# Kernel tuning notes

Hardware: AMD Instinct MI355X
Metric: run time of the kernel (lower is better)

The kernel has to match this reference:

```python
import jax, jax.numpy as jnp
import numpy as np

NUM_HEADS = 16
HEAD_DIM = 64
HIDDEN = NUM_HEADS * HEAD_DIM  # 1024
BATCH, SEQ = 4, 2048


def setup_inputs() -> dict:
    key = jax.random.key(0)
    k1, k2, k3, k4 = jax.random.split(key, 4)
    hidden_states = jax.random.normal(k1, (BATCH, SEQ, HIDDEN), dtype=jnp.float32)
    attention_mask = jnp.arange(SEQ)[None, :] < int(SEQ * 0.9)
    attention_mask = jnp.broadcast_to(attention_mask, (BATCH, SEQ))
    s_in = 1.0 / np.sqrt(HIDDEN)
    Wqkv = jax.random.normal(k2, (HIDDEN, 3 * HIDDEN), dtype=jnp.float32) * s_in
    Wout = jax.random.normal(k3, (HIDDEN, HIDDEN), dtype=jnp.float32) * s_in
    bout = jnp.zeros((HIDDEN,), dtype=jnp.float32)
    return {"hidden_states": hidden_states, "attention_mask": attention_mask,
            "Wqkv": Wqkv, "Wout": Wout, "bout": bout}


def reference(hidden_states, attention_mask, Wqkv, Wout, bout):
    B, S, H = hidden_states.shape
    qkv = hidden_states @ Wqkv  # [B,S,3*H]
    qkv = qkv.reshape(B, S, 3, NUM_HEADS, HEAD_DIM)
    qkv = jnp.transpose(qkv, (2, 0, 3, 1, 4))  # [3,B,nh,S,hd]
    q, k, v = qkv[0], qkv[1], qkv[2]
    scale = 1.0 / jnp.sqrt(jnp.float32(HEAD_DIM))
    attn = jnp.einsum('bhid,bhjd->bhij', q, k) * scale  # [B,nh,S,S]
    bias = jnp.where(attention_mask[:, None, None, :], 0.0,
                     jnp.finfo(jnp.float32).min)
    attn = attn + bias
    attn = jax.nn.softmax(attn, axis=-1)
    out = jnp.einsum('bhij,bhjd->bhid', attn, v)  # [B,nh,S,hd]
    out = jnp.transpose(out, (0, 2, 1, 3)).reshape(B, S, H)
    return out @ Wout + bout
```

## Files before the change

### kernel.cpp

```cpp
#include <hip/hip_runtime.h>


typedef short bh8 __attribute__((ext_vector_type(8)));
typedef short bh4 __attribute__((ext_vector_type(4)));
typedef float f32x4 __attribute__((ext_vector_type(4)));

#define B_ 4
#define S_ 2048
#define NH_ 16
#define HD_ 64
#define H_ 1024

__device__ float g_biasf[B_ * S_];
__device__ int g_tl[B_ * 33];
__device__ unsigned g_act[B_];

__device__ inline short f2bf(float f) {
    unsigned u = __builtin_bit_cast(unsigned, f);
    u = (u + 0x7fffu + ((u >> 16) & 1u)) >> 16;
    return (short)u;
}

__device__ inline unsigned pk2bf(float a, float b) {
#if __has_builtin(__builtin_amdgcn_cvt_pk_bf16_f32)
    auto r = __builtin_amdgcn_cvt_pk_bf16_f32(a, b);
    return __builtin_bit_cast(unsigned, r);
#else
    unsigned ua = __builtin_bit_cast(unsigned, a) + 0x8000u;
    unsigned ub = __builtin_bit_cast(unsigned, b) + 0x8000u;
    return __builtin_amdgcn_perm(ub, ua, 0x07060302);
#endif
}

__global__ void prep_all(const float* __restrict__ hidden, const float* __restrict__ Wqkv,
                         const float* __restrict__ Wout, const int* __restrict__ mask,
                         short* __restrict__ Xbf, short* __restrict__ WqkvT,
                         short* __restrict__ WoutT, float qs) {
    __shared__ float tile[32][33];
    int bi = blockIdx.x, tid = threadIdx.x;

    if (bi < 8192) {
        int i = (bi * 256 + tid) * 4;
        float4 v = *(const float4*)(hidden + i);
        union { short s[4]; unsigned long long u; } r;
        r.s[0] = f2bf(v.x); r.s[1] = f2bf(v.y); r.s[2] = f2bf(v.z); r.s[3] = f2bf(v.w);
        *(unsigned long long*)(Xbf + i) = r.u;
        return;
    }
    if (bi < 12288) {
        const float* in; short* out; int N, qcols, idx;
        if (bi < 11264) { in = Wqkv; out = WqkvT; N = 3 * H_; qcols = H_; idx = bi - 8192;
        } else          { in = Wout; out = WoutT; N = H_;    qcols = 0;  idx = bi - 11264; }
        int xt = (bi < 11264) ? 96 : 32;
        int n0 = (idx % xt) * 32, k0 = (idx / xt) * 32;
        int tx = tid & 31, ty = tid >> 5;
#pragma unroll
        for (int i = 0; i < 32; i += 8)
            tile[ty + i][tx] = in[(long)(k0 + ty + i) * N + n0 + tx];
        __syncthreads();
#pragma unroll
        for (int i = 0; i < 32; i += 8) {
            int n = n0 + ty + i;
            float v = tile[tx][ty + i];
            if (n < qcols) v *= qs;
            out[(long)n * H_ + k0 + tx] = f2bf(v);
        }
        return;
    }
    if (bi < 12320) {
        int i = (bi - 12288) * 256 + tid;
        g_biasf[i] = mask[i] ? 0.0f : -1e30f;
        return;
    }
    {
        int b = bi - 12320;
        if (tid < 64) {
            int t = tid, flag = 0;
            if (t < 32) {
                bool anyA = false, anyM = false;
                for (int i = 0; i < 64; ++i) {
                    int m = mask[b * S_ + t * 64 + i];
                    anyA |= (m != 0); anyM |= (m == 0);
                }
                flag = anyA ? (anyM ? 1 : 2) : 0;
            }
            unsigned long long act = __ballot(flag != 0);
            int pos = __popcll(act & ((1ull << t) - 1ull));
            if (flag) g_tl[b * 33 + 1 + pos] = t | (flag << 16);
            if (t == 0) { g_tl[b * 33] = __popcll(act); g_act[b] = (unsigned)act; }
        }
    }
}

__global__ __launch_bounds__(256, 2) void gemm_bf16(
    const short* __restrict__ A, const short* __restrict__ Bt,
    int M, int N, int K, int mode,
    short* __restrict__ qk, short* __restrict__ vt,
    const float* __restrict__ bias, float* __restrict__ out) {
    __shared__ short smem[128 * 136];
    short* sA[2] = { smem, smem + 4096 };
    short* sB[2] = { smem + 8192, smem + 12288 };
    int tid = threadIdx.x;
    int lane = tid & 63, wid = tid >> 6;
    int quad = lane >> 4, l15 = lane & 15;
    int wy = wid >> 1, wx = wid & 1;
    int m0 = blockIdx.y * 128, n0 = blockIdx.x * 128;
    int rsw = ((l15 >> 1) & 3) << 3;

    if (mode == 0 && n0 >= 1024) {
        int b = m0 >> 11, t0 = (m0 & 2047) >> 6;
        if (((g_act[b] >> t0) & 3u) == 0u) return;
    }

    f32x4 acc[4][4] = {};
    const short* Ag = A + (long)m0 * K;
    const short* Bg = Bt + (long)n0 * K;

    for (int k0 = 0; k0 < K; k0 += 64) {
#pragma unroll
        for (int half = 0; half < 2; ++half) {
#pragma unroll
            for (int i = 0; i < 2; ++i) {
                int flat = i * 256 + tid;
                int r = flat >> 2;
                int c = ((flat & 3) ^ ((flat >> 3) & 3)) << 3;
                __builtin_amdgcn_global_load_lds(
                    (const __attribute__((address_space(1))) void*)(Ag + (long)r * K + k0 + half * 32 + c),
                    (__attribute__((address_space(3))) void*)(sA[half] + i * 2048 + wid * 512),
                    16, 0, 0);
                __builtin_amdgcn_global_load_lds(
                    (const __attribute__((address_space(1))) void*)(Bg + (long)r * K + k0 + half * 32 + c),
                    (__attribute__((address_space(3))) void*)(sB[half] + i * 2048 + wid * 512),
                    16, 0, 0);
            }
        }
        __syncthreads();
#pragma unroll
        for (int half = 0; half < 2; ++half) {
            bh8 af[4], bfr[4];
            int qoff = (quad << 3) ^ rsw;
#pragma unroll
            for (int mi = 0; mi < 4; ++mi)
                af[mi] = *(const bh8*)(sA[half] + (wy * 64 + mi * 16 + l15) * 32 + qoff);
#pragma unroll
            for (int ni = 0; ni < 4; ++ni)
                bfr[ni] = *(const bh8*)(sB[half] + (wx * 64 + ni * 16 + l15) * 32 + qoff);
#pragma unroll
            for (int mi = 0; mi < 4; ++mi)
#pragma unroll
                for (int ni = 0; ni < 4; ++ni)
                    acc[mi][ni] = __builtin_amdgcn_mfma_f32_16x16x32_bf16(af[mi], bfr[ni], acc[mi][ni], 0, 0, 0);
        }
        __syncthreads();
    }

    if (mode == 0) {
        bool isV = (n0 >= 2048);
#pragma unroll
        for (int mi = 0; mi < 4; ++mi)
#pragma unroll
            for (int ni = 0; ni < 4; ++ni) {
                int c = wx * 64 + ni * 16 + l15;
                int rb = wy * 64 + mi * 16 + quad * 4;
                if (isV) {
                    unsigned lo = pk2bf(acc[mi][ni][0], acc[mi][ni][1]);
                    unsigned hi = pk2bf(acc[mi][ni][2], acc[mi][ni][3]);
                    uint2 uu = {lo, hi};
                    *(bh4*)(smem + c * 136 + rb) = __builtin_bit_cast(bh4, uu);
                } else {
#pragma unroll
                    for (int reg = 0; reg < 4; ++reg)
                        smem[(rb + reg) * 136 + c] = f2bf(acc[mi][ni][reg]);
                }
            }
        __syncthreads();
        int b = m0 >> 11, sbase = m0 & 2047;
#pragma unroll
        for (int j = 0; j < 8; ++j) {
            int f = (j * 256 + tid) * 8;
            int i0 = f >> 7, i1 = f & 127;
            bh8 v = *(const bh8*)(smem + i0 * 136 + i1);
            if (isV) {
                int cc = n0 - 2048 + i0;
                int h = cc >> 6, d = cc & 63;
                *(bh8*)(vt + ((long)(b * NH_ + h) * HD_ + d) * S_ + sbase + i1) = v;
            } else {
                *(bh8*)(qk + (long)(m0 + i0) * 2048 + n0 + i1) = v;
            }
        }
    } else {
#pragma unroll
        for (int mi = 0; mi < 4; ++mi)
#pragma unroll
            for (int ni = 0; ni < 4; ++ni) {
                int gc = n0 + wx * 64 + ni * 16 + l15;
                float bv = bias[gc];
#pragma unroll
                for (int reg = 0; reg < 4; ++reg) {
                    int gr = m0 + wy * 64 + mi * 16 + quad * 4 + reg;
                    out[(long)gr * N + gc] = acc[mi][ni][reg] + bv;
                }
            }
    }
}

__global__ __launch_bounds__(256, 2) void attn_fwd(
    const short* __restrict__ QK, const short* __restrict__ Vtw,
    short* __restrict__ Aout) {
    __shared__ short lK[2][64 * 72];
    __shared__ short lV[2][64 * 72];
    int tid = threadIdx.x;
    int lane = tid & 63, w = tid >> 6;
    int quad = lane >> 4, l15 = lane & 15;
    int p = blockIdx.x;
    int b = p >> 4, h = p & 15;
    int qbase = blockIdx.y * 256 + w * 64;

    const short* Kb = QK + (long)b * S_ * 2048 + 1024 + h * HD_;
    const short* Vb = Vtw + (long)p * HD_ * S_;

    int r0 = tid >> 3, g = tid & 7, c = g << 3;
    int voff = (g >> 2) * 32 + (g & 1) * 16 + ((g >> 1) & 1) * 4;
    const short* Kp0 = Kb + (long)r0 * 2048 + c;
    const short* Kp1 = Kp0 + 32l * 2048;
    const short* Vp0 = Vb + (long)r0 * S_ + c;
    const short* Vp1 = Vp0 + 32l * S_;

    bh8 qf[4][2];
#pragma unroll
    for (int mi = 0; mi < 4; ++mi)
#pragma unroll
        for (int ks = 0; ks < 2; ++ks)
            qf[mi][ks] = *(const bh8*)(QK + (long)(b * S_ + qbase + mi * 16 + l15) * 2048
                                       + h * HD_ + ks * 32 + quad * 8);

    f32x4 o[4][4] = {};
    f32x4 ls[4] = {};
    const bh8 ones = {0x3F80, 0x3F80, 0x3F80, 0x3F80, 0x3F80, 0x3F80, 0x3F80, 0x3F80};

    int cnt = g_tl[b * 33];
    int e0 = g_tl[b * 33 + 1];
    int j0 = (e0 & 0xffff) << 6, flag = e0 >> 16;
    bh8 kp[2], vp[2];
    kp[0] = *(const bh8*)(Kp0 + (long)j0 * 2048);
    kp[1] = *(const bh8*)(Kp1 + (long)j0 * 2048);
    vp[0] = *(const bh8*)(Vp0 + j0);
    vp[1] = *(const bh8*)(Vp1 + j0);
    {
        *(bh8*)(lK[0] + r0 * 72 + c) = kp[0];
        *(bh8*)(lK[0] + (r0 + 32) * 72 + c) = kp[1];
        *(bh4*)(lV[0] + r0 * 72 + voff)            = __builtin_shufflevector(vp[0], vp[0], 0, 1, 2, 3);
        *(bh4*)(lV[0] + r0 * 72 + voff + 8)        = __builtin_shufflevector(vp[0], vp[0], 4, 5, 6, 7);
        *(bh4*)(lV[0] + (r0 + 32) * 72 + voff)     = __builtin_shufflevector(vp[1], vp[1], 0, 1, 2, 3);
        *(bh4*)(lV[0] + (r0 + 32) * 72 + voff + 8) = __builtin_shufflevector(vp[1], vp[1], 4, 5, 6, 7);
    }
    int cur = 0;

    for (int it = 0; it < cnt; ++it) {
        __syncthreads();
        bool more = (it + 1 < cnt);
        int nj0 = 0, nflag = 0;
        if (more) {
            int en = g_tl[b * 33 + 2 + it];
            nj0 = (en & 0xffff) << 6; nflag = en >> 16;
            kp[0] = *(const bh8*)(Kp0 + (long)nj0 * 2048);
            kp[1] = *(const bh8*)(Kp1 + (long)nj0 * 2048);
            vp[0] = *(const bh8*)(Vp0 + nj0);
            vp[1] = *(const bh8*)(Vp1 + nj0);
        }
        const short* ck = lK[cur];
        const short* cv = lV[cur];

        bh4 pf[4][4];
#pragma unroll
        for (int nj = 0; nj < 4; ++nj) {
            f32x4 scn[4] = {};
#pragma unroll
            for (int ks = 0; ks < 2; ++ks) {
                bh8 kf = *(const bh8*)(ck + (nj * 16 + l15) * 72 + ks * 32 + quad * 8);
#pragma unroll
                for (int mi = 0; mi < 4; ++mi)
                    scn[mi] = __builtin_amdgcn_mfma_f32_16x16x32_bf16(kf, qf[mi][ks], scn[mi], 0, 0, 0);
            }
            if (flag == 1) {
                f32x4 bb = *(const f32x4*)(g_biasf + b * S_ + j0 + nj * 16 + quad * 4);
#pragma unroll
                for (int mi = 0; mi < 4; ++mi) {
#pragma unroll
                    for (int r = 0; r < 4; ++r) scn[mi][r] += bb[r];
                }
            }
#pragma unroll
            for (int mi = 0; mi < 4; ++mi) {
                unsigned u0 = pk2bf(__builtin_amdgcn_exp2f(scn[mi][0]),
                                    __builtin_amdgcn_exp2f(scn[mi][1]));
                unsigned u1 = pk2bf(__builtin_amdgcn_exp2f(scn[mi][2]),
                                    __builtin_amdgcn_exp2f(scn[mi][3]));
                uint2 uu = {u0, u1};
                pf[nj][mi] = __builtin_bit_cast(bh4, uu);
            }
        }

#pragma unroll
        for (int pr = 0; pr < 2; ++pr) {
            int njA = 2 * pr, njB = 2 * pr + 1;
            bh8 a[4];
#pragma unroll
            for (int mi = 0; mi < 4; ++mi)
                a[mi] = __builtin_shufflevector(pf[njA][mi], pf[njB][mi], 0, 1, 2, 3, 4, 5, 6, 7);
            __builtin_amdgcn_s_setprio(1);
#pragma unroll
            for (int mi = 0; mi < 4; ++mi)
                ls[mi] = __builtin_amdgcn_mfma_f32_16x16x32_bf16(a[mi], ones, ls[mi], 0, 0, 0);
#pragma unroll
            for (int nd = 0; nd < 4; ++nd) {
                bh8 vf = *(const bh8*)(cv + (nd * 16 + l15) * 72 + pr * 32 + quad * 8);
#pragma unroll
                for (int mi = 0; mi < 4; ++mi)
                    o[mi][nd] = __builtin_amdgcn_mfma_f32_16x16x32_bf16(a[mi], vf, o[mi][nd], 0, 0, 0);
            }
            __builtin_amdgcn_s_setprio(0);
        }

        if (more) {
            short* lk = lK[cur ^ 1];
            short* lv = lV[cur ^ 1];
            *(bh8*)(lk + r0 * 72 + c) = kp[0];
            *(bh8*)(lk + (r0 + 32) * 72 + c) = kp[1];
            *(bh4*)(lv + r0 * 72 + voff)            = __builtin_shufflevector(vp[0], vp[0], 0, 1, 2, 3);
            *(bh4*)(lv + r0 * 72 + voff + 8)        = __builtin_shufflevector(vp[0], vp[0], 4, 5, 6, 7);
            *(bh4*)(lv + (r0 + 32) * 72 + voff)     = __builtin_shufflevector(vp[1], vp[1], 0, 1, 2, 3);
            *(bh4*)(lv + (r0 + 32) * 72 + voff + 8) = __builtin_shufflevector(vp[1], vp[1], 4, 5, 6, 7);
        }
        j0 = nj0; flag = nflag; cur ^= 1;
    }

#pragma unroll
    for (int mi = 0; mi < 4; ++mi)
#pragma unroll
        for (int reg = 0; reg < 4; ++reg) {
            float inv = __builtin_amdgcn_rcpf(ls[mi][reg]);
            int s = qbase + mi * 16 + quad * 4 + reg;
#pragma unroll
            for (int nd = 0; nd < 4; ++nd) {
                int col = h * HD_ + nd * 16 + l15;
                Aout[((long)b * S_ + s) * H_ + col] = f2bf(o[mi][nd][reg] * inv);
            }
        }
}

extern "C" void kernel_launch(void* const* d_in, const int* in_sizes, int n_in,
                              void* d_out, int out_size, void* d_ws, size_t ws_size,
                              hipStream_t stream) {
    const float* hidden = (const float*)d_in[0];
    const int* mask = (const int*)d_in[1];
    const float* Wqkv = (const float*)d_in[2];
    const float* Wout = (const float*)d_in[3];
    const float* bout = (const float*)d_in[4];
    float* out = (float*)d_out;

    char* ws = (char*)d_ws;
    const size_t XBF = 0;
    const size_t WQKVT = 16777216;
    const size_t WOUTT = WQKVT + 6291456;
    const size_t QKO = WOUTT + 2097152;
    const size_t VT = QKO + 33554432;

    short* Xbf = (short*)(ws + XBF);
    short* WqkvT = (short*)(ws + WQKVT);
    short* WoutT = (short*)(ws + WOUTT);
    short* QK = (short*)(ws + QKO);
    short* Vt = (short*)(ws + VT);
    short* Aout = Xbf;

    const float Cs = 0.18033688011112042f;

    prep_all<<<dim3(12324), dim3(256), 0, stream>>>(
        hidden, Wqkv, Wout, mask, Xbf, WqkvT, WoutT, Cs);

    gemm_bf16<<<dim3(24, 64), dim3(256), 0, stream>>>(
        Xbf, WqkvT, B_ * S_, 3 * H_, H_, 0, QK, Vt, nullptr, nullptr);

    attn_fwd<<<dim3(64, 8), dim3(256), 0, stream>>>(QK, Vt, Aout);

    gemm_bf16<<<dim3(8, 64), dim3(256), 0, stream>>>(
        Aout, WoutT, B_ * S_, H_, H_, 1, nullptr, nullptr, bout, out);
}
```

Baseline: 252.8 us.

## Process two KV tiles per iteration with quad-buffered LDS in attention

Restructures the attention main loop to handle two 64-key tiles per iteration, using four LDS buffers instead of two and prefetching the next pair of K/V tiles into registers. This halves the number of block-wide barriers and gives more independent MFMA work between synchronisations. In exchange it doubles LDS use (to about 72KB) and raises register pressure from the extra prefetch registers and P fragments, which may reduce occupancy at two blocks per CU.

```diff
diff --git a/kernel.cpp b/kernel.cpp
--- a/kernel.cpp
+++ b/kernel.cpp
@@ -204,11 +204,87 @@
     }
 }
 
+__device__ inline void attn_ldt(const short* Kp0, const short* Kp1,
+                                const short* Vp0, const short* Vp1,
+                                int j0, bh8* kp, bh8* vp) {
+    kp[0] = *(const bh8*)(Kp0 + (long)j0 * 2048);
+    kp[1] = *(const bh8*)(Kp1 + (long)j0 * 2048);
+    vp[0] = *(const bh8*)(Vp0 + j0);
+    vp[1] = *(const bh8*)(Vp1 + j0);
+}
+__device__ inline void attn_stt(short* lk, short* lv, int r0, int c, int voff,
+                                const bh8* kp, const bh8* vp) {
+    *(bh8*)(lk + r0 * 72 + c) = kp[0];
+    *(bh8*)(lk + (r0 + 32) * 72 + c) = kp[1];
+    *(bh4*)(lv + r0 * 72 + voff)            = __builtin_shufflevector(vp[0], vp[0], 0, 1, 2, 3);
+    *(bh4*)(lv + r0 * 72 + voff + 8)        = __builtin_shufflevector(vp[0], vp[0], 4, 5, 6, 7);
+    *(bh4*)(lv + (r0 + 32) * 72 + voff)     = __builtin_shufflevector(vp[1], vp[1], 0, 1, 2, 3);
+    *(bh4*)(lv + (r0 + 32) * 72 + voff + 8) = __builtin_shufflevector(vp[1], vp[1], 4, 5, 6, 7);
+}
+
+__device__ inline void attn_qk(const short* ck, int j0, int flag, const float* biasb,
+                               int quad, int l15, const bh8 (&qf)[4][2],
+                               bh4 (&pf)[4][4]) {
+#pragma unroll
+    for (int nj = 0; nj < 4; ++nj) {
+        f32x4 scn[4] = {};
+#pragma unroll
+        for (int ks = 0; ks < 2; ++ks) {
+            bh8 kf = *(const bh8*)(ck + (nj * 16 + l15) * 72 + ks * 32 + quad * 8);
+#pragma unroll
+            for (int mi = 0; mi < 4; ++mi)
+                scn[mi] = __builtin_amdgcn_mfma_f32_16x16x32_bf16(kf, qf[mi][ks], scn[mi], 0, 0, 0);
+        }
+        if (flag == 1) {
+            f32x4 bb = *(const f32x4*)(biasb + j0 + nj * 16 + quad * 4);
+#pragma unroll
+            for (int mi = 0; mi < 4; ++mi) {
+#pragma unroll
+                for (int r = 0; r < 4; ++r) scn[mi][r] += bb[r];
+            }
+        }
+#pragma unroll
+        for (int mi = 0; mi < 4; ++mi) {
+            unsigned u0 = pk2bf(__builtin_amdgcn_exp2f(scn[mi][0]),
+                                __builtin_amdgcn_exp2f(scn[mi][1]));
+            unsigned u1 = pk2bf(__builtin_amdgcn_exp2f(scn[mi][2]),
+                                __builtin_amdgcn_exp2f(scn[mi][3]));
+            uint2 uu = {u0, u1};
+            pf[nj][mi] = __builtin_bit_cast(bh4, uu);
+        }
+    }
+}
+
+__device__ inline void attn_pv(const short* cv, int quad, int l15,
+                               const bh4 (&pf)[4][4], f32x4 (&o)[4][4], f32x4 (&ls)[4]) {
+    const bh8 ones = {0x3F80, 0x3F80, 0x3F80, 0x3F80, 0x3F80, 0x3F80, 0x3F80, 0x3F80};
+#pragma unroll
+    for (int pr = 0; pr < 2; ++pr) {
+        int njA = 2 * pr, njB = 2 * pr + 1;
+        bh8 a[4];
+#pragma unroll
+        for (int mi = 0; mi < 4; ++mi)
+            a[mi] = __builtin_shufflevector(pf[njA][mi], pf[njB][mi], 0, 1, 2, 3, 4, 5, 6, 7);
+        __builtin_amdgcn_s_setprio(1);
+#pragma unroll
+        for (int mi = 0; mi < 4; ++mi)
+            ls[mi] = __builtin_amdgcn_mfma_f32_16x16x32_bf16(a[mi], ones, ls[mi], 0, 0, 0);
+#pragma unroll
+        for (int nd = 0; nd < 4; ++nd) {
+            bh8 vf = *(const bh8*)(cv + (nd * 16 + l15) * 72 + pr * 32 + quad * 8);
+#pragma unroll
+            for (int mi = 0; mi < 4; ++mi)
+                o[mi][nd] = __builtin_amdgcn_mfma_f32_16x16x32_bf16(a[mi], vf, o[mi][nd], 0, 0, 0);
+        }
+        __builtin_amdgcn_s_setprio(0);
+    }
+}
+
 __global__ __launch_bounds__(256, 2) void attn_fwd(
     const short* __restrict__ QK, const short* __restrict__ Vtw,
     short* __restrict__ Aout) {
-    __shared__ short lK[2][64 * 72];
-    __shared__ short lV[2][64 * 72];
+    __shared__ short lK[4][64 * 72];
+    __shared__ short lV[4][64 * 72];
     int tid = threadIdx.x;
     int lane = tid & 63, w = tid >> 6;
     int quad = lane >> 4, l15 = lane & 15;
@@ -218,6 +294,7 @@
 
     const short* Kb = QK + (long)b * S_ * 2048 + 1024 + h * HD_;
     const short* Vb = Vtw + (long)p * HD_ * S_;
+    const float* biasb = g_biasf + b * S_;
 
     int r0 = tid >> 3, g = tid & 7, c = g << 3;
     int voff = (g >> 2) * 32 + (g & 1) * 16 + ((g >> 1) & 1) * 4;
@@ -236,103 +313,61 @@
 
     f32x4 o[4][4] = {};
     f32x4 ls[4] = {};
-    const bh8 ones = {0x3F80, 0x3F80, 0x3F80, 0x3F80, 0x3F80, 0x3F80, 0x3F80, 0x3F80};
 
     int cnt = g_tl[b * 33];
-    int e0 = g_tl[b * 33 + 1];
-    int j0 = (e0 & 0xffff) << 6, flag = e0 >> 16;
-    bh8 kp[2], vp[2];
-    kp[0] = *(const bh8*)(Kp0 + (long)j0 * 2048);
-    kp[1] = *(const bh8*)(Kp1 + (long)j0 * 2048);
-    vp[0] = *(const bh8*)(Vp0 + j0);
-    vp[1] = *(const bh8*)(Vp1 + j0);
-    {
-        *(bh8*)(lK[0] + r0 * 72 + c) = kp[0];
-        *(bh8*)(lK[0] + (r0 + 32) * 72 + c) = kp[1];
-        *(bh4*)(lV[0] + r0 * 72 + voff)            = __builtin_shufflevector(vp[0], vp[0], 0, 1, 2, 3);
-        *(bh4*)(lV[0] + r0 * 72 + voff + 8)        = __builtin_shufflevector(vp[0], vp[0], 4, 5, 6, 7);
-        *(bh4*)(lV[0] + (r0 + 32) * 72 + voff)     = __builtin_shufflevector(vp[1], vp[1], 0, 1, 2, 3);
-        *(bh4*)(lV[0] + (r0 + 32) * 72 + voff + 8) = __builtin_shufflevector(vp[1], vp[1], 4, 5, 6, 7);
-    }
-    int cur = 0;
-
-    for (int it = 0; it < cnt; ++it) {
-        __syncthreads();
-        bool more = (it + 1 < cnt);
-        int nj0 = 0, nflag = 0;
-        if (more) {
-            int en = g_tl[b * 33 + 2 + it];
-            nj0 = (en & 0xffff) << 6; nflag = en >> 16;
-            kp[0] = *(const bh8*)(Kp0 + (long)nj0 * 2048);
-            kp[1] = *(const bh8*)(Kp1 + (long)nj0 * 2048);
-            vp[0] = *(const bh8*)(Vp0 + nj0);
-            vp[1] = *(const bh8*)(Vp1 + nj0);
-        }
-        const short* ck = lK[cur];
-        const short* cv = lV[cur];
-
-        bh4 pf[4][4];
-#pragma unroll
-        for (int nj = 0; nj < 4; ++nj) {
-            f32x4 scn[4] = {};
-#pragma unroll
-            for (int ks = 0; ks < 2; ++ks) {
-                bh8 kf = *(const bh8*)(ck + (nj * 16 + l15) * 72 + ks * 32 + quad * 8);
-#pragma unroll
-                for (int mi = 0; mi < 4; ++mi)
-                    scn[mi] = __builtin_amdgcn_mfma_f32_16x16x32_bf16(kf, qf[mi][ks], scn[mi], 0, 0, 0);
-            }
-            if (flag == 1) {
-                f32x4 bb = *(const f32x4*)(g_biasf + b * S_ + j0 + nj * 16 + quad * 4);
-#pragma unroll
-                for (int mi = 0; mi < 4; ++mi) {
-#pragma unroll
-                    for (int r = 0; r < 4; ++r) scn[mi][r] += bb[r];
-                }
-            }
-#pragma unroll
-            for (int mi = 0; mi < 4; ++mi) {
-                unsigned u0 = pk2bf(__builtin_amdgcn_exp2f(scn[mi][0]),
-                                    __builtin_amdgcn_exp2f(scn[mi][1]));
-                unsigned u1 = pk2bf(__builtin_amdgcn_exp2f(scn[mi][2]),
-                                    __builtin_amdgcn_exp2f(scn[mi][3]));
-                uint2 uu = {u0, u1};
-                pf[nj][mi] = __builtin_bit_cast(bh4, uu);
-            }
-        }
-
-#pragma unroll
-        for (int pr = 0; pr < 2; ++pr) {
-            int njA = 2 * pr, njB = 2 * pr + 1;
-            bh8 a[4];
-#pragma unroll
-            for (int mi = 0; mi < 4; ++mi)
-                a[mi] = __builtin_shufflevector(pf[njA][mi], pf[njB][mi], 0, 1, 2, 3, 4, 5, 6, 7);
-            __builtin_amdgcn_s_setprio(1);
-#pragma unroll
-            for (int mi = 0; mi < 4; ++mi)
-                ls[mi] = __builtin_amdgcn_mfma_f32_16x16x32_bf16(a[mi], ones, ls[mi], 0, 0, 0);
-#pragma unroll
-            for (int nd = 0; nd < 4; ++nd) {
-                bh8 vf = *(const bh8*)(cv + (nd * 16 + l15) * 72 + pr * 32 + quad * 8);
-#pragma unroll
-                for (int mi = 0; mi < 4; ++mi)
-                    o[mi][nd] = __builtin_amdgcn_mfma_f32_16x16x32_bf16(a[mi], vf, o[mi][nd], 0, 0, 0);
-            }
-            __builtin_amdgcn_s_setprio(0);
-        }
-
-        if (more) {
-            short* lk = lK[cur ^ 1];
-            short* lv = lV[cur ^ 1];
-            *(bh8*)(lk + r0 * 72 + c) = kp[0];
-            *(bh8*)(lk + (r0 + 32) * 72 + c) = kp[1];
-            *(bh4*)(lv + r0 * 72 + voff)            = __builtin_shufflevector(vp[0], vp[0], 0, 1, 2, 3);
-            *(bh4*)(lv + r0 * 72 + voff + 8)        = __builtin_shufflevector(vp[0], vp[0], 4, 5, 6, 7);
-            *(bh4*)(lv + (r0 + 32) * 72 + voff)     = __builtin_shufflevector(vp[1], vp[1], 0, 1, 2, 3);
-            *(bh4*)(lv + (r0 + 32) * 72 + voff + 8) = __builtin_shufflevector(vp[1], vp[1], 4, 5, 6, 7);
-        }
-        j0 = nj0; flag = nflag; cur ^= 1;
+    int npair = cnt >> 1, odd = cnt & 1;
+
+    int j0A = 0, flA = 0, j0B = 0, flB = 0;
+    bh8 kpA[2], vpA[2], kpB[2], vpB[2];
+
+    if (cnt > 0) {
+        int e = g_tl[b * 33 + 1];
+        j0A = (e & 0xffff) << 6; flA = e >> 16;
+        attn_ldt(Kp0, Kp1, Vp0, Vp1, j0A, kpA, vpA);
+        attn_stt(lK[0], lV[0], r0, c, voff, kpA, vpA);
+    }
+    if (cnt > 1) {
+        int e = g_tl[b * 33 + 2];
+        j0B = (e & 0xffff) << 6; flB = e >> 16;
+        attn_ldt(Kp0, Kp1, Vp0, Vp1, j0B, kpB, vpB);
+        attn_stt(lK[1], lV[1], r0, c, voff, kpB, vpB);
+    }
+
+    for (int pp = 0; pp < npair; ++pp) {
+        __syncthreads();
+        int cur = (pp & 1) * 2;
+        int i0 = 2 * pp + 2, i1 = 2 * pp + 3;
+        bool mA = (i0 < cnt), mB = (i1 < cnt);
+        int nj0A = 0, nflA = 0, nj0B = 0, nflB = 0;
+        if (mA) {
+            int e = g_tl[b * 33 + 1 + i0];
+            nj0A = (e & 0xffff) << 6; nflA = e >> 16;
+            attn_ldt(Kp0, Kp1, Vp0, Vp1, nj0A, kpA, vpA);
+        }
+        if (mB) {
+            int e = g_tl[b * 33 + 1 + i1];
+            nj0B = (e & 0xffff) << 6; nflB = e >> 16;
+            attn_ldt(Kp0, Kp1, Vp0, Vp1, nj0B, kpB, vpB);
+        }
+
+        bh4 pfA[4][4], pfB[4][4];
+        attn_qk(lK[cur],     j0A, flA, biasb, quad, l15, qf, pfA);
+        attn_qk(lK[cur + 1], j0B, flB, biasb, quad, l15, qf, pfB);
+        attn_pv(lV[cur],     quad, l15, pfA, o, ls);
+        attn_pv(lV[cur + 1], quad, l15, pfB, o, ls);
+
+        int nb = cur ^ 2;
+        if (mA) attn_stt(lK[nb],     lV[nb],     r0, c, voff, kpA, vpA);
+        if (mB) attn_stt(lK[nb + 1], lV[nb + 1], r0, c, voff, kpB, vpB);
+        j0A = nj0A; flA = nflA; j0B = nj0B; flB = nflB;
+    }
+
+    if (odd) {
+        __syncthreads();
+        int tb = (npair & 1) * 2;
+        bh4 pfT[4][4];
+        attn_qk(lK[tb], j0A, flA, biasb, quad, l15, qf, pfT);
+        attn_pv(lV[tb], quad, l15, pfT, o, ls);
     }
 
 #pragma unroll
```

After: 310.3 us. +22.8%, slower.
